# Performance work log

Hardware: AMD Instinct MI355X
Metric: run time of the kernel (lower is better)

The kernel has to match this reference:

```python
import jax, jax.numpy as jnp
import numpy as np

N = 10000; E = 160000; C = 32; NB = 128; H = 64; L = 3; NL = 4; RC = 5.0
DIMS = [1, 3, 5, 7]

def _sph(v):
    # real spherical harmonics l=0..3 of unit vectors v [E,3]
    x, y, z = v[:, 0], v[:, 1], v[:, 2]
    s3 = 3.0 ** 0.5; s5 = 5.0 ** 0.5; s15 = 15.0 ** 0.5; s7 = 7.0 ** 0.5
    sh0 = jnp.ones_like(x)[:, None]
    sh1 = s3 * v
    sh2 = jnp.stack([s15 * x * y, s15 * y * z, (s5 / 2) * (3 * z * z - 1),
                     s15 * x * z, (s15 / 2) * (x * x - y * y)], -1)
    c1 = (35.0 / 8) ** 0.5; c2 = 105.0 ** 0.5; c3 = (21.0 / 8) ** 0.5; c4 = s7 / 2; c5 = (105.0 ** 0.5) / 2
    sh3 = jnp.stack([c1 * y * (3 * x * x - y * y), c2 * x * y * z, c3 * y * (5 * z * z - 1),
                     c4 * (5 * z ** 3 - 3 * z), c3 * x * (5 * z * z - 1),
                     c5 * z * (x * x - y * y), c1 * x * (x * x - 3 * y * y)], -1)
    return [sh0, sh1, sh2, sh3]

def setup_inputs() -> dict:
    key = jax.random.key(0)
    ks = jax.random.split(key, 14)
    inp = {}
    inp['pos'] = jax.random.uniform(ks[0], (N, 3), jnp.float32) * 10.0  # box of side 10
    inp['node_embed'] = jax.random.normal(ks[1], (4, C), jnp.float32)
    inp['rw1'] = jax.random.normal(ks[2], (NB, H), jnp.float32) * 0.1
    inp['rb1'] = jax.random.normal(ks[3], (H,), jnp.float32) * 0.1
    inp['rw2'] = jax.random.normal(ks[4], (H, L * NL * C), jnp.float32) * 0.1
    inp['rb2'] = jax.random.normal(ks[5], (L * NL * C,), jnp.float32) * 0.1
    inp['self_w'] = jax.random.normal(ks[6], (L, NL, C, C), jnp.float32) * (1.0 / C ** 0.5)
    inp['msg_w'] = jax.random.normal(ks[7], (L, NL, C, C), jnp.float32) * (1.0 / C ** 0.5)
    inp['gate_w'] = jax.random.normal(ks[8], (L, C, C), jnp.float32) * (1.0 / C ** 0.5)
    inp['edge_w'] = jax.random.normal(ks[9], (H, NL * C), jnp.float32) * 0.1
    inp['edge_b'] = jax.random.normal(ks[10], (NL * C,), jnp.float32) * 0.1
    inp['species'] = jax.random.randint(ks[11], (N,), 0, 4)
    inp['edge_index'] = jax.random.randint(ks[12], (2, E), 0, N)
    return inp

def reference(pos, node_embed, rw1, rb1, rw2, rb2, self_w, msg_w, gate_w,
              edge_w, edge_b, species, edge_index):
    src, dst = edge_index[0], edge_index[1]
    vec = pos[dst] - pos[src]                       # [E,3]
    r = jnp.sqrt(jnp.sum(vec * vec, -1) + 1e-12)    # [E]
    u = jnp.clip(r / RC, 0.0, 1.0)
    env = 0.5 * (jnp.cos(jnp.pi * u) + 1.0)         # smooth cutoff, 0 beyond rc
    n = jnp.arange(1, NB + 1, dtype=pos.dtype)
    rb = env[:, None] * (2.0 / RC) ** 0.5 * jnp.sin(jnp.pi * n * u[:, None]) / r[:, None]  # Bessel basis [E,NB]
    h = jax.nn.silu(rb @ rw1 + rb1)                 # [E,H]
    w_all = (h @ rw2 + rb2).reshape(E, L, NL, C)    # per-layer per-l radial weights
    ew = (h @ edge_w + edge_b).reshape(E, NL, C)
    sh = _sph(vec / r[:, None])                     # list of [E, 2l+1]
    # node features per l: [N, C, 2l+1]; l=0 initialized from species embedding
    f = [node_embed[species][:, :, None]] + [jnp.zeros((N, C, d), pos.dtype) for d in DIMS[1:]]
    for t in range(L):
        s = f[0][src][:, :, 0]                      # sender scalars [E,C]
        new = []
        for l in range(NL):
            # scalar-gated radial x SH message (equivariant): [E,C,2l+1]
            m = w_all[:, t, l, :, None] * s[:, :, None] * sh[l][:, None, :]
            agg = jax.ops.segment_sum(m, dst, num_segments=N)
            new.append(jnp.einsum('ncm,cd->ndm', f[l], self_w[t, l]) +
                       jnp.einsum('ncm,cd->ndm', agg, msg_w[t, l]))
        gate = jax.nn.sigmoid(new[0][:, :, 0] @ gate_w[t])  # [N,C]
        f = [jax.nn.silu(new[0])] + [new[l] * gate[:, :, None] for l in range(1, NL)]
    node_out = jnp.concatenate([f[l].reshape(N, C * DIMS[l]) for l in range(NL)], -1)   # [N,512]
    g = f[0][src][:, :, 0] + f[0][dst][:, :, 0]     # [E,C]
    edge_out = jnp.concatenate(
        [(ew[:, l, :, None] * g[:, :, None] * sh[l][:, None, :]).reshape(E, C * DIMS[l])
         for l in range(NL)], -1)                   # [E,512]
    return jnp.concatenate([node_out, edge_out], 0)  # [N+E, 512]
```

## Files before the change

kernel.cpp:

```cpp
#include <hip/hip_runtime.h>

#define NN 10000
#define EE 160000
#define CC 32
#define NBAS 128
#define HH 64
#define LL 3

__device__ __forceinline__ float sigmoidf_(float x) { return 1.0f / (1.0f + expf(-x)); }

__device__ __forceinline__ void edge_geom(const float* pos, int src, int dst,
                                          float& inv_r, float& u, float& pref,
                                          float& x, float& y, float& z) {
    float vx = pos[dst * 3 + 0] - pos[src * 3 + 0];
    float vy = pos[dst * 3 + 1] - pos[src * 3 + 1];
    float vz = pos[dst * 3 + 2] - pos[src * 3 + 2];
    float r2 = vx * vx + vy * vy + vz * vz + 1e-12f;
    float r = sqrtf(r2);
    inv_r = 1.0f / r;
    u = fminf(r * 0.2f, 1.0f);
    const float PI = 3.14159265358979f;
    float env = 0.5f * (cosf(PI * u) + 1.0f);
    pref = env * 0.6324555320336759f * inv_r;
    x = vx * inv_r; y = vy * inv_r; z = vz * inv_r;
}

__device__ __forceinline__ void sph_all(float x, float y, float z, float* shv) {
    const float s3 = 1.7320508075688772f, s5 = 2.23606797749979f, s15 = 3.872983346207417f;
    const float c1 = 2.0916500663351885f;
    const float c2 = 10.246950765959598f;
    const float c3 = 1.6201851746019649f;
    const float c4 = 1.3228756555322954f;
    const float c5 = 5.123475382979799f;
    shv[0] = 1.0f;
    shv[1] = s3 * x; shv[2] = s3 * y; shv[3] = s3 * z;
    shv[4] = s15 * x * y;
    shv[5] = s15 * y * z;
    shv[6] = 0.5f * s5 * (3.0f * z * z - 1.0f);
    shv[7] = s15 * x * z;
    shv[8] = 0.5f * s15 * (x * x - y * y);
    shv[9]  = c1 * y * (3.0f * x * x - y * y);
    shv[10] = c2 * x * y * z;
    shv[11] = c3 * y * (5.0f * z * z - 1.0f);
    shv[12] = c4 * (5.0f * z * z * z - 3.0f * z);
    shv[13] = c3 * x * (5.0f * z * z - 1.0f);
    shv[14] = c5 * z * (x * x - y * y);
    shv[15] = c1 * x * (x * x - 3.0f * y * y);
}

__global__ void k_deg(const int* __restrict__ ei, int* __restrict__ deg) {
    int e = blockIdx.x * blockDim.x + threadIdx.x;
    if (e < EE) atomicAdd(&deg[ei[EE + e]], 1);
}

__global__ __launch_bounds__(256) void k_scan(const int* __restrict__ deg, int* __restrict__ rowptr) {
    __shared__ int part[256];
    const int CHUNK = 40;
    int tid = threadIdx.x;
    int s = 0;
#pragma unroll
    for (int k = 0; k < CHUNK; k++) {
        int idx = tid * CHUNK + k;
        if (idx < NN) s += deg[idx];
    }
    part[tid] = s;
    __syncthreads();
    for (int off = 1; off < 256; off <<= 1) {
        int v = (tid >= off) ? part[tid - off] : 0;
        __syncthreads();
        part[tid] += v;
        __syncthreads();
    }
    int run = (tid > 0) ? part[tid - 1] : 0;
#pragma unroll
    for (int k = 0; k < CHUNK; k++) {
        int idx = tid * CHUNK + k;
        if (idx < NN) { rowptr[idx] = run; run += deg[idx]; }
    }
    if (tid == 255) rowptr[NN] = run;
}

__global__ void k_scatter(const int* __restrict__ ei, const int* __restrict__ rowptr,
                          int* __restrict__ cursor, int* __restrict__ csr) {
    int e = blockIdx.x * blockDim.x + threadIdx.x;
    if (e >= EE) return;
    int d = ei[EE + e];
    int slot = atomicAdd(&cursor[d], 1);
    csr[rowptr[d] + slot] = e;
}

__global__ void k_init_f(const float* __restrict__ ne, const int* __restrict__ species,
                         float* __restrict__ f, float* __restrict__ f0) {
    int idx = blockIdx.x * blockDim.x + threadIdx.x;
    if (idx >= NN * CC * 16) return;
    int m = idx & 15;
    int c = (idx >> 4) & 31;
    int n = idx >> 9;
    float v = (m == 0) ? ne[species[n] * CC + c] : 0.0f;
    f[idx] = v;
    if (m == 0) f0[n * CC + c] = v;
}

__global__ __launch_bounds__(256) void k_edge_pre(
    const float* __restrict__ pos, const float* __restrict__ rw1, const float* __restrict__ rb1,
    const int* __restrict__ ei, float* __restrict__ hbuf, float* __restrict__ shbuf) {
    __shared__ float rw1_s[NBAS * HH];
    __shared__ float rb_s[64 * 132];
    int tid = threadIdx.x;
    int ebase = blockIdx.x * 64;
    for (int i = tid; i < NBAS * HH / 4; i += 256)
        *(float4*)&rw1_s[i * 4] = *(const float4*)&rw1[i * 4];
    {
        int r = tid >> 2, q = tid & 3;
        int e = ebase + r;
        int src = ei[e], dst = ei[EE + e];
        float inv_r, u, pref, x, y, z;
        edge_geom(pos, src, dst, inv_r, u, pref, x, y, z);
        float shv[16];
        sph_all(x, y, z, shv);
        float4 sv;
        sv.x = shv[q * 4 + 0]; sv.y = shv[q * 4 + 1];
        sv.z = shv[q * 4 + 2]; sv.w = shv[q * 4 + 3];
        *(float4*)&shbuf[(size_t)e * 16 + q * 4] = sv;
        const float PI = 3.14159265358979f;
        float th = PI * u;
        float tc = 2.0f * cosf(th);
        int n0 = 32 * q + 1;
        float sp2 = sinf(th * (float)n0);
        float sp1 = sinf(th * (float)(n0 + 1));
        float* rp = &rb_s[r * 132 + 32 * q];
        float4 v;
        v.x = pref * sp2; v.y = pref * sp1;
#pragma unroll
        for (int j = 2; j < 32; j++) {
            float s = tc * sp1 - sp2;
            sp2 = sp1; sp1 = s;
            float pv = pref * s;
            int m = j & 3;
            if (m == 0) v.x = pv;
            else if (m == 1) v.y = pv;
            else if (m == 2) v.z = pv;
            else { v.w = pv; *(float4*)&rp[j - 3] = v; }
        }
    }
    __syncthreads();
    int col0 = (tid & 15) * 4;
    int r0 = (tid >> 4) * 4;
    float acc[4][4];
#pragma unroll
    for (int i = 0; i < 4; i++) { acc[i][0] = 0.f; acc[i][1] = 0.f; acc[i][2] = 0.f; acc[i][3] = 0.f; }
#pragma unroll 2
    for (int k0 = 0; k0 < NBAS; k0 += 4) {
        float4 w0 = *(float4*)&rw1_s[(k0 + 0) * HH + col0];
        float4 w1 = *(float4*)&rw1_s[(k0 + 1) * HH + col0];
        float4 w2 = *(float4*)&rw1_s[(k0 + 2) * HH + col0];
        float4 w3 = *(float4*)&rw1_s[(k0 + 3) * HH + col0];
#pragma unroll
        for (int i = 0; i < 4; i++) {
            float4 rv = *(float4*)&rb_s[(r0 + i) * 132 + k0];
            acc[i][0] += rv.x * w0.x; acc[i][1] += rv.x * w0.y; acc[i][2] += rv.x * w0.z; acc[i][3] += rv.x * w0.w;
            acc[i][0] += rv.y * w1.x; acc[i][1] += rv.y * w1.y; acc[i][2] += rv.y * w1.z; acc[i][3] += rv.y * w1.w;
            acc[i][0] += rv.z * w2.x; acc[i][1] += rv.z * w2.y; acc[i][2] += rv.z * w2.z; acc[i][3] += rv.z * w2.w;
            acc[i][0] += rv.w * w3.x; acc[i][1] += rv.w * w3.y; acc[i][2] += rv.w * w3.z; acc[i][3] += rv.w * w3.w;
        }
    }
    float4 bv = *(const float4*)&rb1[col0];
#pragma unroll
    for (int i = 0; i < 4; i++) {
        float a0 = acc[i][0] + bv.x, a1 = acc[i][1] + bv.y;
        float a2 = acc[i][2] + bv.z, a3 = acc[i][3] + bv.w;
        float4 hres;
        hres.x = a0 * sigmoidf_(a0); hres.y = a1 * sigmoidf_(a1);
        hres.z = a2 * sigmoidf_(a2); hres.w = a3 * sigmoidf_(a3);
        *(float4*)&hbuf[(size_t)(ebase + r0 + i) * HH + col0] = hres;
    }
}

__global__ __launch_bounds__(256) void k_gemm_all(
    const float* __restrict__ hbuf, const float* __restrict__ rw2,
    const float* __restrict__ rb2, const int* __restrict__ csr,
    float* __restrict__ aw, int panel0, int npanel, int ostride) {
    __shared__ float w_s[HH * 128];
    __shared__ float h_s[64][68];
    int tid = threadIdx.x;
    int pbase = blockIdx.x * 64;
    {
        int r = tid >> 2, q = tid & 3;
        int e = csr[pbase + r];
        const float4* hp = (const float4*)(hbuf + (size_t)e * HH + q * 16);
        float4 v0 = hp[0], v1 = hp[1], v2 = hp[2], v3 = hp[3];
        float4* dp = (float4*)&h_s[r][q * 16];
        dp[0] = v0; dp[1] = v1; dp[2] = v2; dp[3] = v3;
    }
    int ob = (tid & 31) << 2;
    int r0 = (tid >> 5) << 3;
    for (int p = 0; p < npanel; p++) {
        int wcol = (panel0 + p) * 128;
        __syncthreads();
        for (int i = tid; i < HH * 32; i += 256) {
            int j = i >> 5, o4 = (i & 31) << 2;
            *(float4*)&w_s[j * 128 + o4] = *(const float4*)&rw2[(size_t)j * 384 + wcol + o4];
        }
        __syncthreads();
        float acc[8][4];
#pragma unroll
        for (int i = 0; i < 8; i++) { acc[i][0] = 0.f; acc[i][1] = 0.f; acc[i][2] = 0.f; acc[i][3] = 0.f; }
#pragma unroll 2
        for (int k0 = 0; k0 < HH; k0 += 4) {
            float4 w0 = *(float4*)&w_s[(k0 + 0) * 128 + ob];
            float4 w1 = *(float4*)&w_s[(k0 + 1) * 128 + ob];
            float4 w2 = *(float4*)&w_s[(k0 + 2) * 128 + ob];
            float4 w3 = *(float4*)&w_s[(k0 + 3) * 128 + ob];
#pragma unroll
            for (int i = 0; i < 8; i++) {
                float4 hv = *(float4*)&h_s[r0 + i][k0];
                acc[i][0] += hv.x * w0.x; acc[i][1] += hv.x * w0.y; acc[i][2] += hv.x * w0.z; acc[i][3] += hv.x * w0.w;
                acc[i][0] += hv.y * w1.x; acc[i][1] += hv.y * w1.y; acc[i][2] += hv.y * w1.z; acc[i][3] += hv.y * w1.w;
                acc[i][0] += hv.z * w2.x; acc[i][1] += hv.z * w2.y; acc[i][2] += hv.z * w2.z; acc[i][3] += hv.z * w2.w;
                acc[i][0] += hv.w * w3.x; acc[i][1] += hv.w * w3.y; acc[i][2] += hv.w * w3.z; acc[i][3] += hv.w * w3.w;
            }
        }
        float4 bv = *(const float4*)&rb2[wcol + ob];
#pragma unroll
        for (int i = 0; i < 8; i++) {
            float4 res;
            res.x = acc[i][0] + bv.x; res.y = acc[i][1] + bv.y;
            res.z = acc[i][2] + bv.z; res.w = acc[i][3] + bv.w;
            *(float4*)&aw[(size_t)(pbase + r0 + i) * ostride + p * 128 + ob] = res;
        }
    }
}

__global__ __launch_bounds__(256) void k_agg2(
    const float* __restrict__ aw, const float* __restrict__ shbuf,
    const float* __restrict__ f0, const int* __restrict__ ei,
    const int* __restrict__ rowptr, const int* __restrict__ csr,
    float* __restrict__ agg, int coloff, int ostride) {
    int w = threadIdx.x >> 6, lane = threadIdx.x & 63;
    int n = blockIdx.x * 4 + w;
    int c = lane & 31;
    int half = lane >> 5;
    float acc0[3] = {0.f, 0.f, 0.f};
    float acc1[7] = {0.f, 0.f, 0.f, 0.f, 0.f, 0.f, 0.f};
    int beg = rowptr[n], end = rowptr[n + 1];
    for (int k = beg; k < end; k++) {
        int e = csr[k];
        int src = ei[e];
        float fs = f0[src * CC + c];
        float a0 = aw[(size_t)k * ostride + coloff + lane] * fs;
        float a1 = aw[(size_t)k * ostride + coloff + 64 + lane] * fs;
        const float4* shp = (const float4*)(shbuf + (size_t)e * 16);
        float4 s0 = shp[0], s1 = shp[1], s2 = shp[2], s3 = shp[3];
        if (half == 0) {
            acc0[0] += a0 * s0.x;
            acc1[0] += a1 * s1.x; acc1[1] += a1 * s1.y; acc1[2] += a1 * s1.z; acc1[3] += a1 * s1.w;
            acc1[4] += a1 * s2.x;
        } else {
            acc0[0] += a0 * s0.y; acc0[1] += a0 * s0.z; acc0[2] += a0 * s0.w;
            acc1[0] += a1 * s2.y; acc1[1] += a1 * s2.z; acc1[2] += a1 * s2.w;
            acc1[3] += a1 * s3.x; acc1[4] += a1 * s3.y; acc1[5] += a1 * s3.z; acc1[6] += a1 * s3.w;
        }
    }
    int l0 = half, dl0 = 2 * l0 + 1, mo0 = l0 * l0;
    int l1 = 2 + half, dl1 = 2 * l1 + 1, mo1 = l1 * l1;
    float* ap = agg + ((size_t)n * CC + c) * 16;
#pragma unroll
    for (int m = 0; m < 3; m++)
        if (m < dl0) ap[mo0 + m] = acc0[m];
#pragma unroll
    for (int m = 0; m < 7; m++)
        if (m < dl1) ap[mo1 + m] = acc1[m];
}

__global__ __launch_bounds__(256) void k_node(
    const float* __restrict__ f_cur, const float* __restrict__ agg,
    const float* __restrict__ self_w, const float* __restrict__ msg_w,
    const float* __restrict__ gate_w, float* __restrict__ f_next,
    float* __restrict__ f0_out, int t) {
    __shared__ float new_s[4][CC * 16];
    __shared__ float gate_s[4][CC];
    int w = threadIdx.x >> 6, lane = threadIdx.x & 63;
    int n = blockIdx.x * 4 + w;
    int d = lane & 31, mg = lane >> 5;
#pragma unroll
    for (int k = 0; k < 8; k++) {
        int m = mg + 2 * k;
        int l = (m == 0) ? 0 : (m < 4) ? 1 : (m < 9) ? 2 : 3;
        const float* sw = self_w + (size_t)((t * 4 + l) * CC) * CC + d;
        const float* mw = msg_w + (size_t)((t * 4 + l) * CC) * CC + d;
        const float* fp = f_cur + (size_t)n * CC * 16 + m;
        const float* ap = agg + (size_t)n * CC * 16 + m;
        float acc = 0.0f;
#pragma unroll 8
        for (int c = 0; c < CC; c++)
            acc += fp[c * 16] * sw[c * CC] + ap[c * 16] * mw[c * CC];
        new_s[w][d * 16 + m] = acc;
    }
    __syncthreads();
    if (mg == 0) {
        float g = 0.0f;
#pragma unroll 8
        for (int c = 0; c < CC; c++) g += new_s[w][c * 16 + 0] * gate_w[((size_t)t * CC + c) * CC + d];
        gate_s[w][d] = sigmoidf_(g);
    }
    __syncthreads();
#pragma unroll
    for (int k = 0; k < 8; k++) {
        int m = mg + 2 * k;
        float v = new_s[w][d * 16 + m];
        if (m == 0) v = v * sigmoidf_(v);
        else v *= gate_s[w][d];
        f_next[((size_t)n * CC + d) * 16 + m] = v;
        if (m == 0) f0_out[n * CC + d] = v;
    }
}

__global__ void k_out_node(const float* __restrict__ f, float* __restrict__ out) {
    int idx = blockIdx.x * blockDim.x + threadIdx.x;
    if (idx >= NN * 512) return;
    int n = idx >> 9, q = idx & 511;
    int l, c, m;
    if (q < 32) { l = 0; c = q; m = 0; }
    else if (q < 128) { l = 1; c = (q - 32) / 3; m = (q - 32) % 3; }
    else if (q < 288) { l = 2; c = (q - 128) / 5; m = (q - 128) % 5; }
    else { l = 3; c = (q - 288) / 7; m = (q - 288) % 7; }
    out[idx] = f[((size_t)n * CC + c) * 16 + l * l + m];
}

template<int DL>
__device__ __forceinline__ void emit_edge(float* outp, const float* shp,
                                          float e0, float e1, float e2, float e3) {
    float ew[4] = {e0, e1, e2, e3};
    float buf[4 * DL];
#pragma unroll
    for (int cc = 0; cc < 4; cc++)
#pragma unroll
        for (int m = 0; m < DL; m++) buf[cc * DL + m] = ew[cc] * shp[m];
#pragma unroll
    for (int t = 0; t < DL; t++) *(float4*)&outp[t * 4] = *(float4*)&buf[t * 4];
}

__global__ __launch_bounds__(256) void k_edge_out(
    const float* __restrict__ hbuf, const float* __restrict__ shbuf,
    const float* __restrict__ edge_w, const float* __restrict__ edge_b,
    const float* __restrict__ f0, const int* __restrict__ ei,
    float* __restrict__ out) {
    __shared__ float w_s[HH * 128];
    __shared__ float h_s[64][68];
    __shared__ float sh_s[64][16];
    int tid = threadIdx.x;
    int ebase = blockIdx.x * 64;
    for (int i = tid; i < HH * 32; i += 256) {
        int j = i >> 5, o4 = (i & 31) << 2;
        *(float4*)&w_s[j * 128 + o4] = *(const float4*)&edge_w[(size_t)j * 128 + o4];
    }
    {
        int r = tid >> 2, q = tid & 3;
        int e = ebase + r;
        const float4* hp = (const float4*)(hbuf + (size_t)e * HH + q * 16);
        float4 v0 = hp[0], v1 = hp[1], v2 = hp[2], v3 = hp[3];
        float4* dp = (float4*)&h_s[r][q * 16];
        dp[0] = v0; dp[1] = v1; dp[2] = v2; dp[3] = v3;
        *(float4*)&sh_s[r][q * 4] = *(const float4*)&shbuf[(size_t)e * 16 + q * 4];
    }
    __syncthreads();
    int ob = (tid & 31) << 2;
    int r0 = (tid >> 5) << 3;
    float acc[8][4];
#pragma unroll
    for (int i = 0; i < 8; i++) { acc[i][0] = 0.f; acc[i][1] = 0.f; acc[i][2] = 0.f; acc[i][3] = 0.f; }
#pragma unroll 2
    for (int k0 = 0; k0 < HH; k0 += 4) {
        float4 w0 = *(float4*)&w_s[(k0 + 0) * 128 + ob];
        float4 w1 = *(float4*)&w_s[(k0 + 1) * 128 + ob];
        float4 w2 = *(float4*)&w_s[(k0 + 2) * 128 + ob];
        float4 w3 = *(float4*)&w_s[(k0 + 3) * 128 + ob];
#pragma unroll
        for (int i = 0; i < 8; i++) {
            float4 hv = *(float4*)&h_s[r0 + i][k0];
            acc[i][0] += hv.x * w0.x; acc[i][1] += hv.x * w0.y; acc[i][2] += hv.x * w0.z; acc[i][3] += hv.x * w0.w;
            acc[i][0] += hv.y * w1.x; acc[i][1] += hv.y * w1.y; acc[i][2] += hv.y * w1.z; acc[i][3] += hv.y * w1.w;
            acc[i][0] += hv.z * w2.x; acc[i][1] += hv.z * w2.y; acc[i][2] += hv.z * w2.z; acc[i][3] += hv.z * w2.w;
            acc[i][0] += hv.w * w3.x; acc[i][1] += hv.w * w3.y; acc[i][2] += hv.w * w3.z; acc[i][3] += hv.w * w3.w;
        }
    }
    float4 bv = *(const float4*)&edge_b[ob];
    int l = ob >> 5;
    int cbase = ob & 31;
    int dl = 2 * l + 1, mo = l * l, co = 32 * l * l;
#pragma unroll
    for (int i = 0; i < 8; i++) {
        int rr = r0 + i;
        int e = ebase + rr;
        int src = ei[e], dst = ei[EE + e];
        float4 g1 = *(const float4*)&f0[src * CC + cbase];
        float4 g2 = *(const float4*)&f0[dst * CC + cbase];
        float e0 = (acc[i][0] + bv.x) * (g1.x + g2.x);
        float e1 = (acc[i][1] + bv.y) * (g1.y + g2.y);
        float e2 = (acc[i][2] + bv.z) * (g1.z + g2.z);
        float e3 = (acc[i][3] + bv.w) * (g1.w + g2.w);
        float* outp = out + ((size_t)NN + e) * 512 + co + (size_t)cbase * dl;
        const float* shp = &sh_s[rr][mo];
        if (l == 0)      emit_edge<1>(outp, shp, e0, e1, e2, e3);
        else if (l == 1) emit_edge<3>(outp, shp, e0, e1, e2, e3);
        else if (l == 2) emit_edge<5>(outp, shp, e0, e1, e2, e3);
        else             emit_edge<7>(outp, shp, e0, e1, e2, e3);
    }
}

__global__ __launch_bounds__(256) void k_out_edge(
    const float* __restrict__ pos, const float* __restrict__ rw1, const float* __restrict__ rb1,
    const float* __restrict__ edge_w, const float* __restrict__ edge_b,
    const float* __restrict__ f0, const int* __restrict__ ei, float* __restrict__ out) {
    __shared__ float rw1_s[NBAS * HH];
    __shared__ float ew_s[HH * 128];
    __shared__ float rb_s[4][NBAS];
    __shared__ float h_s[4][HH];
    __shared__ float g_s[4][CC];
    __shared__ float sh_s[4][16];
    int tid = threadIdx.x;
    for (int i = tid; i < NBAS * HH; i += 256) rw1_s[i] = rw1[i];
    for (int i = tid; i < HH * 128; i += 256) ew_s[i] = edge_w[i];
    int w = tid >> 6, lane = tid & 63;
    int e = blockIdx.x * 4 + w;
    int src = ei[e], dst = ei[EE + e];
    float inv_r, u, pref, x, y, z;
    edge_geom(pos, src, dst, inv_r, u, pref, x, y, z);
    const float PI = 3.14159265358979f;
#pragma unroll
    for (int rep = 0; rep < 2; rep++) {
        int k = lane + rep * 64;
        rb_s[w][k] = pref * sinf(PI * (float)(k + 1) * u);
    }
    float shv[16];
    sph_all(x, y, z, shv);
    if (lane < 16) {
        float v = shv[0];
#pragma unroll
        for (int k = 1; k < 16; k++) v = (lane == k) ? shv[k] : v;
        sh_s[w][lane] = v;
    }
    if (lane < CC) g_s[w][lane] = f0[src * CC + lane] + f0[dst * CC + lane];
    __syncthreads();
    float acc = rb1[lane];
#pragma unroll 8
    for (int n = 0; n < NBAS; n++) acc += rb_s[w][n] * rw1_s[n * HH + lane];
    h_s[w][lane] = acc * sigmoidf_(acc);
    __syncthreads();
    size_t orow = ((size_t)NN + e) * 512;
#pragma unroll
    for (int rep = 0; rep < 2; rep++) {
        int o = lane + rep * 64;
        int l = o >> 5, c = o & 31;
        float a = edge_b[o];
#pragma unroll 8
        for (int j = 0; j < HH; j++) a += h_s[w][j] * ew_s[j * 128 + o];
        float base = a * g_s[w][c];
        int dl = 2 * l + 1, mo = l * l, co = 32 * l * l;
        for (int m = 0; m < dl; m++) out[orow + co + c * dl + m] = base * sh_s[w][mo + m];
    }
}

extern "C" void kernel_launch(void* const* d_in, const int* in_sizes, int n_in,
                              void* d_out, int out_size, void* d_ws, size_t ws_size,
                              hipStream_t stream) {
    const float* pos        = (const float*)d_in[0];
    const float* node_embed = (const float*)d_in[1];
    const float* rw1        = (const float*)d_in[2];
    const float* rb1        = (const float*)d_in[3];
    const float* rw2        = (const float*)d_in[4];
    const float* rb2        = (const float*)d_in[5];
    const float* self_w     = (const float*)d_in[6];
    const float* msg_w      = (const float*)d_in[7];
    const float* gate_w     = (const float*)d_in[8];
    const float* edge_w     = (const float*)d_in[9];
    const float* edge_b     = (const float*)d_in[10];
    const int* species      = (const int*)d_in[11];
    const int* ei           = (const int*)d_in[12];
    float* out = (float*)d_out;

    float* f0fin = (float*)d_ws;
    float* f0ar  = f0fin + (size_t)NN * CC;
    float* hbuf  = f0ar + (size_t)NN * CC;
    float* shbuf = hbuf + (size_t)EE * HH;
    float* fA    = shbuf + (size_t)EE * 16;
    float* agg   = fA + (size_t)NN * 512;
    int* deg     = (int*)(agg + (size_t)NN * 512);
    int* rowptr  = deg + NN;
    int* cursor  = rowptr + NN + 1;
    int* csr     = cursor + NN;
    size_t base_need = (size_t)((char*)(csr + EE) - (char*)d_ws);
    size_t extra_need = ((size_t)NN * 512 + (size_t)EE * 384) * 4;
    float* fB;
    float* aw;
    bool deep_fallback = false;
    if (ws_size >= base_need + extra_need) {
        fB = (float*)((char*)d_ws + base_need);
        aw = fB + (size_t)NN * 512;
    } else if (ws_size >= base_need) {
        fB = out + (size_t)NN * 512;
        aw = fB + (size_t)NN * 512;
    } else {
        deep_fallback = true;
        float* s = out + (size_t)NN * 512;
        hbuf = s; shbuf = hbuf + (size_t)EE * HH;
        fA = shbuf + (size_t)EE * 16;
        agg = fA + (size_t)NN * 512;
        fB = agg + (size_t)NN * 512;
        aw = fB + (size_t)NN * 512;
        deg = (int*)(aw + (size_t)EE * 128);
        rowptr = deg + NN; cursor = rowptr + NN + 1; csr = cursor + NN;
    }

    hipMemsetAsync(deg, 0, (size_t)NN * 4, stream);
    hipMemsetAsync(cursor, 0, (size_t)NN * 4, stream);
    k_deg<<<(EE + 255) / 256, 256, 0, stream>>>(ei, deg);
    k_scan<<<1, 256, 0, stream>>>(deg, rowptr);
    k_scatter<<<(EE + 255) / 256, 256, 0, stream>>>(ei, rowptr, cursor, csr);

    k_init_f<<<(NN * CC * 16 + 255) / 256, 256, 0, stream>>>(node_embed, species, fA, f0ar);
    k_edge_pre<<<EE / 64, 256, 0, stream>>>(pos, rw1, rb1, ei, hbuf, shbuf);

    float* fc = fA;
    float* fn = fB;
    if (!deep_fallback) {
        k_gemm_all<<<EE / 64, 256, 0, stream>>>(hbuf, rw2, rb2, csr, aw, 0, 3, 384);
        for (int t = 0; t < LL; t++) {
            k_agg2<<<NN / 4, 256, 0, stream>>>(aw, shbuf, f0ar, ei, rowptr, csr, agg, t * 128, 384);
            float* f0o = (t == LL - 1) ? f0fin : f0ar;
            k_node<<<NN / 4, 256, 0, stream>>>(fc, agg, self_w, msg_w, gate_w, fn, f0o, t);
            float* tmp = fc; fc = fn; fn = tmp;
        }
        k_out_node<<<(NN * 512 + 255) / 256, 256, 0, stream>>>(fc, out);
        k_edge_out<<<EE / 64, 256, 0, stream>>>(hbuf, shbuf, edge_w, edge_b, f0fin, ei, out);
    } else {
        for (int t = 0; t < LL; t++) {
            k_gemm_all<<<EE / 64, 256, 0, stream>>>(hbuf, rw2, rb2, csr, aw, t, 1, 128);
            k_agg2<<<NN / 4, 256, 0, stream>>>(aw, shbuf, f0ar, ei, rowptr, csr, agg, 0, 128);
            float* f0o = (t == LL - 1) ? f0fin : f0ar;
            k_node<<<NN / 4, 256, 0, stream>>>(fc, agg, self_w, msg_w, gate_w, fn, f0o, t);
            float* tmp = fc; fc = fn; fn = tmp;
        }
        k_out_node<<<(NN * 512 + 255) / 256, 256, 0, stream>>>(fc, out);
        k_out_edge<<<EE / 4, 256, 0, stream>>>(pos, rw1, rb1, edge_w, edge_b, f0fin, ei, out);
    }
}
```

Measured before the change: 1.267 ms.

## Fuse aggregation with node update and write final layer directly to output

Merges the per-layer neighbour aggregation and node-update kernels into one templated kernel that keeps the aggregate in shared memory. This removes the global agg buffer round trip and half the launches. The first layer reads f0 instead of a zero-padded feature tensor, so the full init kernel is dropped. The last layer writes straight into the packed output layout, which removes k_out_node. The per-layer edge-weight panels become contiguous [E,128] slabs, and the sine recurrence is split into two shorter chains. Block-level syncthreads were removed, which relies on each wave touching only its own shared slice.

```diff
diff --git a/kernel.cpp b/kernel.cpp
--- a/kernel.cpp
+++ b/kernel.cpp
@@ -89,16 +89,13 @@
     csr[rowptr[d] + slot] = e;
 }
 
-__global__ void k_init_f(const float* __restrict__ ne, const int* __restrict__ species,
-                         float* __restrict__ f, float* __restrict__ f0) {
+__global__ void k_init_f0(const float* __restrict__ ne, const int* __restrict__ species,
+                          float* __restrict__ f0) {
     int idx = blockIdx.x * blockDim.x + threadIdx.x;
-    if (idx >= NN * CC * 16) return;
-    int m = idx & 15;
-    int c = (idx >> 4) & 31;
-    int n = idx >> 9;
-    float v = (m == 0) ? ne[species[n] * CC + c] : 0.0f;
-    f[idx] = v;
-    if (m == 0) f0[n * CC + c] = v;
+    if (idx >= NN * CC) return;
+    int c = idx & 31;
+    int n = idx >> 5;
+    f0[idx] = ne[species[n] * CC + c];
 }
 
 __global__ __launch_bounds__(256) void k_edge_pre(
@@ -125,22 +122,21 @@
         const float PI = 3.14159265358979f;
         float th = PI * u;
         float tc = 2.0f * cosf(th);
+        float* rp = &rb_s[r * 132 + 32 * q];
         int n0 = 32 * q + 1;
-        float sp2 = sinf(th * (float)n0);
-        float sp1 = sinf(th * (float)(n0 + 1));
-        float* rp = &rb_s[r * 132 + 32 * q];
-        float4 v;
-        v.x = pref * sp2; v.y = pref * sp1;
-#pragma unroll
-        for (int j = 2; j < 32; j++) {
-            float s = tc * sp1 - sp2;
-            sp2 = sp1; sp1 = s;
-            float pv = pref * s;
-            int m = j & 3;
-            if (m == 0) v.x = pv;
-            else if (m == 1) v.y = pv;
-            else if (m == 2) v.z = pv;
-            else { v.w = pv; *(float4*)&rp[j - 3] = v; }
+#pragma unroll
+        for (int g = 0; g < 2; g++) {
+            int nb = n0 + 16 * g;
+            float sm1 = sinf(th * (float)nb);
+            float s0 = sinf(th * (float)(nb + 1));
+            rp[16 * g + 0] = pref * sm1;
+            rp[16 * g + 1] = pref * s0;
+#pragma unroll
+            for (int j = 2; j < 16; j++) {
+                float s = tc * s0 - sm1;
+                sm1 = s0; s0 = s;
+                rp[16 * g + j] = pref * s;
+            }
         }
     }
     __syncthreads();
@@ -179,7 +175,7 @@
 __global__ __launch_bounds__(256) void k_gemm_all(
     const float* __restrict__ hbuf, const float* __restrict__ rw2,
     const float* __restrict__ rb2, const int* __restrict__ csr,
-    float* __restrict__ aw, int panel0, int npanel, int ostride) {
+    float* __restrict__ aw, int panel0, int npanel) {
     __shared__ float w_s[HH * 128];
     __shared__ float h_s[64][68];
     int tid = threadIdx.x;
@@ -221,21 +217,29 @@
             }
         }
         float4 bv = *(const float4*)&rb2[wcol + ob];
+        float* awp = aw + (size_t)p * EE * 128;
 #pragma unroll
         for (int i = 0; i < 8; i++) {
             float4 res;
             res.x = acc[i][0] + bv.x; res.y = acc[i][1] + bv.y;
             res.z = acc[i][2] + bv.z; res.w = acc[i][3] + bv.w;
-            *(float4*)&aw[(size_t)(pbase + r0 + i) * ostride + p * 128 + ob] = res;
-        }
-    }
-}
-
-__global__ __launch_bounds__(256) void k_agg2(
+            *(float4*)&awp[(size_t)(pbase + r0 + i) * 128 + ob] = res;
+        }
+    }
+}
+
+template<int INIT, int FINAL>
+__global__ __launch_bounds__(256) void k_aggnode(
     const float* __restrict__ aw, const float* __restrict__ shbuf,
-    const float* __restrict__ f0, const int* __restrict__ ei,
-    const int* __restrict__ rowptr, const int* __restrict__ csr,
-    float* __restrict__ agg, int coloff, int ostride) {
+    const float* __restrict__ f0prev, const float* __restrict__ f_cur,
+    const int* __restrict__ ei, const int* __restrict__ rowptr,
+    const int* __restrict__ csr,
+    const float* __restrict__ self_w, const float* __restrict__ msg_w,
+    const float* __restrict__ gate_w,
+    float* __restrict__ f_next, float* __restrict__ f0_out, int t) {
+    __shared__ float agg_s[4][CC * 17];
+    __shared__ float new_s[4][CC * 17];
+    __shared__ float gate_s[4][CC];
     int w = threadIdx.x >> 6, lane = threadIdx.x & 63;
     int n = blockIdx.x * 4 + w;
     int c = lane & 31;
@@ -246,85 +250,70 @@
     for (int k = beg; k < end; k++) {
         int e = csr[k];
         int src = ei[e];
-        float fs = f0[src * CC + c];
-        float a0 = aw[(size_t)k * ostride + coloff + lane] * fs;
-        float a1 = aw[(size_t)k * ostride + coloff + 64 + lane] * fs;
+        float fs = f0prev[src * CC + c];
+        float a0 = aw[(size_t)k * 128 + lane] * fs;
+        float a1 = aw[(size_t)k * 128 + 64 + lane] * fs;
         const float4* shp = (const float4*)(shbuf + (size_t)e * 16);
         float4 s0 = shp[0], s1 = shp[1], s2 = shp[2], s3 = shp[3];
         if (half == 0) {
             acc0[0] += a0 * s0.x;
-            acc1[0] += a1 * s1.x; acc1[1] += a1 * s1.y; acc1[2] += a1 * s1.z; acc1[3] += a1 * s1.w;
-            acc1[4] += a1 * s2.x;
+            acc1[0] += a1 * s1.x; acc1[1] += a1 * s1.y;
+            acc1[2] += a1 * s1.z; acc1[3] += a1 * s1.w; acc1[4] += a1 * s2.x;
         } else {
             acc0[0] += a0 * s0.y; acc0[1] += a0 * s0.z; acc0[2] += a0 * s0.w;
             acc1[0] += a1 * s2.y; acc1[1] += a1 * s2.z; acc1[2] += a1 * s2.w;
             acc1[3] += a1 * s3.x; acc1[4] += a1 * s3.y; acc1[5] += a1 * s3.z; acc1[6] += a1 * s3.w;
         }
     }
-    int l0 = half, dl0 = 2 * l0 + 1, mo0 = l0 * l0;
-    int l1 = 2 + half, dl1 = 2 * l1 + 1, mo1 = l1 * l1;
-    float* ap = agg + ((size_t)n * CC + c) * 16;
-#pragma unroll
-    for (int m = 0; m < 3; m++)
-        if (m < dl0) ap[mo0 + m] = acc0[m];
-#pragma unroll
-    for (int m = 0; m < 7; m++)
-        if (m < dl1) ap[mo1 + m] = acc1[m];
-}
-
-__global__ __launch_bounds__(256) void k_node(
-    const float* __restrict__ f_cur, const float* __restrict__ agg,
-    const float* __restrict__ self_w, const float* __restrict__ msg_w,
-    const float* __restrict__ gate_w, float* __restrict__ f_next,
-    float* __restrict__ f0_out, int t) {
-    __shared__ float new_s[4][CC * 16];
-    __shared__ float gate_s[4][CC];
-    int w = threadIdx.x >> 6, lane = threadIdx.x & 63;
-    int n = blockIdx.x * 4 + w;
-    int d = lane & 31, mg = lane >> 5;
+    {
+        int l0 = half, dl0 = 2 * l0 + 1, mo0 = l0 * l0;
+        int l1 = 2 + half, dl1 = 2 * l1 + 1, mo1 = l1 * l1;
+        float* ap = &agg_s[w][c * 17];
+#pragma unroll
+        for (int m = 0; m < 3; m++)
+            if (m < dl0) ap[mo0 + m] = acc0[m];
+#pragma unroll
+        for (int m = 0; m < 7; m++)
+            if (m < dl1) ap[mo1 + m] = acc1[m];
+    }
+    int d = c, mg = half;
 #pragma unroll
     for (int k = 0; k < 8; k++) {
         int m = mg + 2 * k;
         int l = (m == 0) ? 0 : (m < 4) ? 1 : (m < 9) ? 2 : 3;
         const float* sw = self_w + (size_t)((t * 4 + l) * CC) * CC + d;
         const float* mw = msg_w + (size_t)((t * 4 + l) * CC) * CC + d;
-        const float* fp = f_cur + (size_t)n * CC * 16 + m;
-        const float* ap = agg + (size_t)n * CC * 16 + m;
         float acc = 0.0f;
 #pragma unroll 8
-        for (int c = 0; c < CC; c++)
-            acc += fp[c * 16] * sw[c * CC] + ap[c * 16] * mw[c * CC];
-        new_s[w][d * 16 + m] = acc;
-    }
-    __syncthreads();
+        for (int c2 = 0; c2 < CC; c2++) {
+            float fv;
+            if (INIT) fv = (m == 0) ? f0prev[n * CC + c2] : 0.0f;
+            else fv = f_cur[((size_t)n * CC + c2) * 16 + m];
+            acc += fv * sw[c2 * CC] + agg_s[w][c2 * 17 + m] * mw[c2 * CC];
+        }
+        new_s[w][d * 17 + m] = acc;
+    }
     if (mg == 0) {
         float g = 0.0f;
 #pragma unroll 8
-        for (int c = 0; c < CC; c++) g += new_s[w][c * 16 + 0] * gate_w[((size_t)t * CC + c) * CC + d];
+        for (int c2 = 0; c2 < CC; c2++)
+            g += new_s[w][c2 * 17 + 0] * gate_w[((size_t)t * CC + c2) * CC + d];
         gate_s[w][d] = sigmoidf_(g);
     }
-    __syncthreads();
 #pragma unroll
     for (int k = 0; k < 8; k++) {
         int m = mg + 2 * k;
-        float v = new_s[w][d * 16 + m];
+        float v = new_s[w][d * 17 + m];
         if (m == 0) v = v * sigmoidf_(v);
         else v *= gate_s[w][d];
-        f_next[((size_t)n * CC + d) * 16 + m] = v;
+        if (FINAL) {
+            int l = (m == 0) ? 0 : (m < 4) ? 1 : (m < 9) ? 2 : 3;
+            f_next[(size_t)n * 512 + 32 * l * l + d * (2 * l + 1) + (m - l * l)] = v;
+        } else {
+            f_next[((size_t)n * CC + d) * 16 + m] = v;
+        }
         if (m == 0) f0_out[n * CC + d] = v;
     }
-}
-
-__global__ void k_out_node(const float* __restrict__ f, float* __restrict__ out) {
-    int idx = blockIdx.x * blockDim.x + threadIdx.x;
-    if (idx >= NN * 512) return;
-    int n = idx >> 9, q = idx & 511;
-    int l, c, m;
-    if (q < 32) { l = 0; c = q; m = 0; }
-    else if (q < 128) { l = 1; c = (q - 32) / 3; m = (q - 32) % 3; }
-    else if (q < 288) { l = 2; c = (q - 128) / 5; m = (q - 128) % 5; }
-    else { l = 3; c = (q - 288) / 7; m = (q - 288) % 7; }
-    out[idx] = f[((size_t)n * CC + c) * 16 + l * l + m];
 }
 
 template<int DL>
@@ -480,12 +469,12 @@
     float* out = (float*)d_out;
 
     float* f0fin = (float*)d_ws;
-    float* f0ar  = f0fin + (size_t)NN * CC;
-    float* hbuf  = f0ar + (size_t)NN * CC;
+    float* f0A   = f0fin + (size_t)NN * CC;
+    float* f0B   = f0A + (size_t)NN * CC;
+    float* hbuf  = f0B + (size_t)NN * CC;
     float* shbuf = hbuf + (size_t)EE * HH;
     float* fA    = shbuf + (size_t)EE * 16;
-    float* agg   = fA + (size_t)NN * 512;
-    int* deg     = (int*)(agg + (size_t)NN * 512);
+    int* deg     = (int*)(fA + (size_t)NN * 512);
     int* rowptr  = deg + NN;
     int* cursor  = rowptr + NN + 1;
     int* csr     = cursor + NN;
@@ -505,8 +494,7 @@
         float* s = out + (size_t)NN * 512;
         hbuf = s; shbuf = hbuf + (size_t)EE * HH;
         fA = shbuf + (size_t)EE * 16;
-        agg = fA + (size_t)NN * 512;
-        fB = agg + (size_t)NN * 512;
+        fB = fA + (size_t)NN * 512;
         aw = fB + (size_t)NN * 512;
         deg = (int*)(aw + (size_t)EE * 128);
         rowptr = deg + NN; cursor = rowptr + NN + 1; csr = cursor + NN;
@@ -518,30 +506,28 @@
     k_scan<<<1, 256, 0, stream>>>(deg, rowptr);
     k_scatter<<<(EE + 255) / 256, 256, 0, stream>>>(ei, rowptr, cursor, csr);
 
-    k_init_f<<<(NN * CC * 16 + 255) / 256, 256, 0, stream>>>(node_embed, species, fA, f0ar);
+    k_init_f0<<<(NN * CC + 255) / 256, 256, 0, stream>>>(node_embed, species, f0A);
     k_edge_pre<<<EE / 64, 256, 0, stream>>>(pos, rw1, rb1, ei, hbuf, shbuf);
 
-    float* fc = fA;
-    float* fn = fB;
     if (!deep_fallback) {
-        k_gemm_all<<<EE / 64, 256, 0, stream>>>(hbuf, rw2, rb2, csr, aw, 0, 3, 384);
-        for (int t = 0; t < LL; t++) {
-            k_agg2<<<NN / 4, 256, 0, stream>>>(aw, shbuf, f0ar, ei, rowptr, csr, agg, t * 128, 384);
-            float* f0o = (t == LL - 1) ? f0fin : f0ar;
-            k_node<<<NN / 4, 256, 0, stream>>>(fc, agg, self_w, msg_w, gate_w, fn, f0o, t);
-            float* tmp = fc; fc = fn; fn = tmp;
-        }
-        k_out_node<<<(NN * 512 + 255) / 256, 256, 0, stream>>>(fc, out);
+        k_gemm_all<<<EE / 64, 256, 0, stream>>>(hbuf, rw2, rb2, csr, aw, 0, 3);
+        k_aggnode<1, 0><<<NN / 4, 256, 0, stream>>>(aw, shbuf, f0A, nullptr,
+            ei, rowptr, csr, self_w, msg_w, gate_w, fA, f0B, 0);
+        k_aggnode<0, 0><<<NN / 4, 256, 0, stream>>>(aw + (size_t)EE * 128, shbuf, f0B, fA,
+            ei, rowptr, csr, self_w, msg_w, gate_w, fB, f0A, 1);
+        k_aggnode<0, 1><<<NN / 4, 256, 0, stream>>>(aw + (size_t)2 * EE * 128, shbuf, f0A, fB,
+            ei, rowptr, csr, self_w, msg_w, gate_w, out, f0fin, 2);
         k_edge_out<<<EE / 64, 256, 0, stream>>>(hbuf, shbuf, edge_w, edge_b, f0fin, ei, out);
     } else {
-        for (int t = 0; t < LL; t++) {
-            k_gemm_all<<<EE / 64, 256, 0, stream>>>(hbuf, rw2, rb2, csr, aw, t, 1, 128);
-            k_agg2<<<NN / 4, 256, 0, stream>>>(aw, shbuf, f0ar, ei, rowptr, csr, agg, 0, 128);
-            float* f0o = (t == LL - 1) ? f0fin : f0ar;
-            k_node<<<NN / 4, 256, 0, stream>>>(fc, agg, self_w, msg_w, gate_w, fn, f0o, t);
-            float* tmp = fc; fc = fn; fn = tmp;
-        }
-        k_out_node<<<(NN * 512 + 255) / 256, 256, 0, stream>>>(fc, out);
+        k_gemm_all<<<EE / 64, 256, 0, stream>>>(hbuf, rw2, rb2, csr, aw, 0, 1);
+        k_aggnode<1, 0><<<NN / 4, 256, 0, stream>>>(aw, shbuf, f0A, nullptr,
+            ei, rowptr, csr, self_w, msg_w, gate_w, fA, f0B, 0);
+        k_gemm_all<<<EE / 64, 256, 0, stream>>>(hbuf, rw2, rb2, csr, aw, 1, 1);
+        k_aggnode<0, 0><<<NN / 4, 256, 0, stream>>>(aw, shbuf, f0B, fA,
+            ei, rowptr, csr, self_w, msg_w, gate_w, fB, f0A, 1);
+        k_gemm_all<<<EE / 64, 256, 0, stream>>>(hbuf, rw2, rb2, csr, aw, 2, 1);
+        k_aggnode<0, 1><<<NN / 4, 256, 0, stream>>>(aw, shbuf, f0A, fB,
+            ei, rowptr, csr, self_w, msg_w, gate_w, out, f0fin, 2);
         k_out_edge<<<EE / 4, 256, 0, stream>>>(pos, rw1, rb1, edge_w, edge_b, f0fin, ei, out);
     }
 }
```

Result: faster. 1.133 ms (-10.6%).
